# Optimization experiments

Hardware: AMD Instinct MI355X
Metric: run time of the kernel (lower is better)

The kernel has to match this reference:

```python
import jax, jax.numpy as jnp
import numpy as np

B = 16  # graphs per batch; equal-sized graphs per level

def _knn_interpolate(x, pos, pos_skip, k):
    # x: [Ns, C] source feats, pos: [Ns,3], pos_skip: [Nt,3]; B equal-sized graphs.
    Ns, C = x.shape
    Nt = pos_skip.shape[0]
    xs = x.reshape(B, Ns // B, C)
    ps = pos.reshape(B, Ns // B, 3)
    pt = pos_skip.reshape(B, Nt // B, 3)
    def per_graph(xb, pb, qb):
        # squared pairwise distance [nt, ns]
        d2 = (jnp.sum(qb * qb, -1)[:, None] + jnp.sum(pb * pb, -1)[None, :]
              - 2.0 * (qb @ pb.T))
        neg, idx = jax.lax.top_k(-d2, k)          # k smallest distances
        w = 1.0 / jnp.clip(-neg, 1e-16)           # inverse-distance weights [nt,k]
        xg = xb[idx]                               # gather [nt,k,C]
        return jnp.sum(w[..., None] * xg, 1) / jnp.sum(w, 1)[..., None]
    y = jax.vmap(per_graph)(xs, ps, pt)
    return y.reshape(Nt, C)

def _lin(x, W, b):
    return x @ W.T + b

def setup_inputs() -> dict:
    key = jax.random.key(0)
    ks = jax.random.split(key, 24)
    n3, n2, n1, n0 = 1024, 4096, 16384, 65536
    def rn(k, shape, scale=1.0):
        return (jax.random.normal(k, shape, dtype=jnp.float32) * scale)
    inp = {
        'x': rn(ks[0], (n3, 256)),
        'pos': rn(ks[1], (n3, 3)),
        'batch': jnp.repeat(jnp.arange(B), n3 // B),
        'x_skip2': rn(ks[2], (n2, 128)),
        'pos_skip2': rn(ks[3], (n2, 3)),
        'batch2': jnp.repeat(jnp.arange(B), n2 // B),
        'x_skip1': rn(ks[4], (n1, 64)),
        'pos_skip1': rn(ks[5], (n1, 3)),
        'batch1': jnp.repeat(jnp.arange(B), n1 // B),
        'x_skip0': rn(ks[6], (n0, 3)),
        'pos_skip0': rn(ks[7], (n0, 3)),
        'batch0': jnp.repeat(jnp.arange(B), n0 // B),
        # MLP([384,128,128])
        'W3a': rn(ks[8], (128, 384), 384 ** -0.5), 'b3a': jnp.zeros((128,), jnp.float32),
        'W3b': rn(ks[9], (128, 128), 128 ** -0.5), 'b3b': jnp.zeros((128,), jnp.float32),
        # MLP([192,64,64])
        'W2a': rn(ks[10], (64, 192), 192 ** -0.5), 'b2a': jnp.zeros((64,), jnp.float32),
        'W2b': rn(ks[11], (64, 64), 64 ** -0.5), 'b2b': jnp.zeros((64,), jnp.float32),
        # MLP([67,64,64,3])
        'W1a': rn(ks[12], (64, 67), 67 ** -0.5), 'b1a': jnp.zeros((64,), jnp.float32),
        'W1b': rn(ks[13], (64, 64), 64 ** -0.5), 'b1b': jnp.zeros((64,), jnp.float32),
        'W1c': rn(ks[14], (3, 64), 64 ** -0.5), 'b1c': jnp.zeros((3,), jnp.float32),
    }
    return inp

def reference(x, pos, batch, x_skip2, pos_skip2, batch2, x_skip1, pos_skip1, batch1,
              x_skip0, pos_skip0, batch0, W3a, b3a, W3b, b3b, W2a, b2a, W2b, b2b,
              W1a, b1a, W1b, b1b, W1c, b1c):
    # propagate3: k=4, MLP([384,128,128], Tanh, plain last layer)
    h = _knn_interpolate(x, pos, pos_skip2, 4)
    h = jnp.concatenate([h, x_skip2], axis=1)
    h = _lin(jnp.tanh(_lin(h, W3a, b3a)), W3b, b3b)
    # propagate2: k=8, MLP([192,64,64])
    h = _knn_interpolate(h, pos_skip2, pos_skip1, 8)
    h = jnp.concatenate([h, x_skip1], axis=1)
    h = _lin(jnp.tanh(_lin(h, W2a, b2a)), W2b, b2b)
    # propagate1: k=16, MLP([67,64,64,3])
    h = _knn_interpolate(h, pos_skip1, pos_skip0, 16)
    h = jnp.concatenate([h, x_skip0], axis=1)
    h = _lin(jnp.tanh(_lin(jnp.tanh(_lin(h, W1a, b1a)), W1b, b1b)), W1c, b1c)
    return h
```

## Files before the change

kernel.cpp:

```cpp
#include <hip/hip_runtime.h>
#include <math.h>

#define DEV __device__ __forceinline__

typedef unsigned long long u64;
typedef unsigned u32;

DEV u32 fmap(float f) {
    u32 b = __float_as_uint(f);
    return b ^ (u32)(((int)b >> 31) | 0x80000000);
}
DEV float funmap(u32 m) {
    u32 b = (m & 0x80000000u) ? (m ^ 0x80000000u) : ~m;
    return __uint_as_float(b);
}
DEV u32 umin_(u32 a, u32 b) { return __builtin_elementwise_min(a, b); }
DEV u32 umax_(u32 a, u32 b) { return __builtin_elementwise_max(a, b); }

DEV int lane_rank(u64 mask) {
    return (int)__builtin_amdgcn_mbcnt_hi((u32)(mask >> 32),
               __builtin_amdgcn_mbcnt_lo((u32)mask, 0u));
}

DEV float pnorm2(float x, float y, float z) {
    return __fmaf_rn(x, x, __fmaf_rn(y, y, __fmul_rn(z, z)));
}
DEV float qdot(float qx, float qy, float qz, float px, float py, float pz) {
    return __fmaf_rn(qx, px, __fmaf_rn(qy, py, __fmul_rn(qz, pz)));
}
DEV float dist2_core(float qq, float pp, float qp) {
    return __fadd_rn(__fadd_rn(qq, pp), __fmul_rn(-2.f, qp));
}
DEV float dist2(float qx, float qy, float qz, float qq,
                float px, float py, float pz) {
    return dist2_core(qq, pnorm2(px, py, pz), qdot(qx, qy, qz, px, py, pz));
}
DEV float wgt(float d2) { return __builtin_amdgcn_rcpf(fmaxf(d2, 1e-16f)); }

template<int N>
DEV void bitonic_sort(u32 v[N]) {
    #pragma unroll
    for (int k = 2; k <= N; k <<= 1) {
        #pragma unroll
        for (int j = k >> 1; j > 0; j >>= 1) {
            #pragma unroll
            for (int i = 0; i < N; ++i) {
                const int l = i ^ j;
                if (l > i) {
                    const u32 lo = umin_(v[i], v[l]);
                    const u32 hi = umax_(v[i], v[l]);
                    const bool up = ((i & k) == 0);
                    v[i] = up ? lo : hi;
                    v[l] = up ? hi : lo;
                }
            }
        }
    }
}
template<int N>
DEV void bitonic_cleanup(u32 v[N]) {
    #pragma unroll
    for (int j = N >> 1; j > 0; j >>= 1) {
        #pragma unroll
        for (int i = 0; i < N; ++i) {
            const int l = i ^ j;
            if (l > i) {
                const u32 lo = umin_(v[i], v[l]);
                v[l] = umax_(v[i], v[l]);
                v[i] = lo;
            }
        }
    }
}

template<int K, int NSRC, int LOG_TPG, int TPT>
__global__ __launch_bounds__(256) void knn_select(
    const float* __restrict__ pos_s, const float* __restrict__ pos_t,
    u32* __restrict__ Fout)
{
    constexpr int TPB = 256 / TPT;
    constexpr int SL  = NSRC / TPT;
    constexpr int NB  = SL / K;
    constexpr int STRIDE = TPT * K + 1;
    __shared__ float4 sp[NSRC];
    __shared__ u32 lists[TPB * STRIDE];

    const int tid = threadIdx.x;
    const int w = tid / TPT, sub = tid % TPT;
    const int t = blockIdx.x * TPB + w;
    const int g = t >> LOG_TPG, sbase = g * NSRC;

    for (int i = tid; i < NSRC; i += 256) {
        const float* p = pos_s + (size_t)(sbase + i) * 3;
        const float px = p[0], py = p[1], pz = p[2];
        sp[i] = make_float4(px, py, pz, pnorm2(px, py, pz));
    }
    __syncthreads();

    const float qx = pos_t[t*3+0], qy = pos_t[t*3+1], qz = pos_t[t*3+2];
    const float qq = pnorm2(qx, qy, qz);

    u32 r[K];
    #pragma unroll
    for (int j = 0; j < K; ++j) r[j] = 0xFFFFFFFFu;

    for (int b = 0; b < NB; ++b) {
        u32 c[K];
        #pragma unroll
        for (int j = 0; j < K; ++j) {
            const float4 p = sp[(b * K + j) * TPT + sub];
            c[j] = fmap(dist2_core(qq, p.w, qdot(qx, qy, qz, p.x, p.y, p.z)));
        }
        bitonic_sort<K>(c);
        u32 m[K];
        #pragma unroll
        for (int i = 0; i < K; ++i) m[i] = umin_(r[i], c[K-1-i]);
        bitonic_cleanup<K>(m);
        #pragma unroll
        for (int i = 0; i < K; ++i) r[i] = m[i];
    }

    u32* Lw = lists + w * STRIDE;
    #pragma unroll
    for (int j = 0; j < K; ++j) Lw[sub * K + j] = r[j];
    __syncthreads();

    if (sub == 0) {
        u32 h[TPT]; int idx[TPT];
        #pragma unroll
        for (int l = 0; l < TPT; ++l) { h[l] = Lw[l*K]; idx[l] = 1; }
        u32 F = 0;
        #pragma unroll
        for (int step = 0; step < K; ++step) {
            u32 m = h[0];
            #pragma unroll
            for (int l = 1; l < TPT; ++l) m = umin_(m, h[l]);
            F = m;
            if (step < K - 1) {
                bool done = false;
                #pragma unroll
                for (int l = 0; l < TPT; ++l) {
                    if (!done && h[l] == m) {
                        h[l] = (idx[l] < K) ? Lw[l*K + idx[l]] : 0xFFFFFFFFu;
                        ++idx[l];
                        done = true;
                    }
                }
            }
        }
        Fout[t] = F;
    }
}


__global__ __launch_bounds__(512) void knn1_gather(
    const float* __restrict__ xsrc, const float* __restrict__ pos_s,
    const float* __restrict__ pos_t, const float* __restrict__ x_skip,
    const u32* __restrict__ Fbuf, float* __restrict__ out)
{
    constexpr int K = 16, M = 16;
    __shared__ float4 sp[1024];
    __shared__ int2 srw[8 * K];
    const int lane = threadIdx.x & 63;
    const int wv = threadIdx.x >> 6;
    const int t = blockIdx.x * 8 + wv;
    const int g = (blockIdx.x * 8) >> 12;
    const int sbase = g << 10;

    for (int i = threadIdx.x; i < 1024; i += 512) {
        const float* p = pos_s + (size_t)(sbase + i) * 3;
        const float px = p[0], py = p[1], pz = p[2];
        sp[i] = make_float4(px, py, pz, pnorm2(px, py, pz));
    }
    __syncthreads();

    const float qx = pos_t[t*3+0], qy = pos_t[t*3+1], qz = pos_t[t*3+2];
    const float qq = pnorm2(qx, qy, qz);
    float fd[M];
    #pragma unroll
    for (int m = 0; m < M; ++m) {
        const float4 p = sp[lane + m*64];
        fd[m] = dist2_core(qq, p.w, qdot(qx, qy, qz, p.x, p.y, p.z));
    }
    const float Fd = funmap(Fbuf[t]);
    const int base = wv * K;

    int bl = 0, bt = 0; int tr[M];
    #pragma unroll
    for (int m = 0; m < M; ++m) {
        const u64 mlm = __ballot(fd[m] < Fd);
        const u64 mtm = __ballot(fd[m] == Fd);
        if (fd[m] < Fd) {
            const int slot = bl + lane_rank(mlm);
            srw[base + slot] = make_int2(__float_as_int(wgt(fd[m])),
                                         sbase + lane + m*64);
        }
        tr[m] = bt + lane_rank(mtm);
        bl += (int)__popcll(mlm);
        bt += (int)__popcll(mtm);
    }
    const int nless = bl, need = K - nless;
    const float wtie = wgt(Fd);
    #pragma unroll
    for (int m = 0; m < M; ++m) {
        if (fd[m] == Fd && tr[m] < need) {
            srw[base + nless + tr[m]] = make_int2(__float_as_int(wtie),
                                                  sbase + lane + m*64);
        }
    }
    __syncthreads();

    float wsum = 0.f, y = 0.f;
    #pragma unroll
    for (int j = 0; j < K; ++j) {
        const int2 rw = srw[base + j];
        const float w = __int_as_float(rw.x);
        wsum += w;
        y += w * xsrc[(size_t)rw.y * 64 + lane];
    }
    out[t*67 + lane] = y * (1.f / wsum);
    if (lane < 3) out[t*67 + 64 + lane] = x_skip[t*3 + lane];
}

__global__ __launch_bounds__(512) void knn2_gather(
    const float* __restrict__ xsrc, const float* __restrict__ pos_s,
    const float* __restrict__ pos_t, const float* __restrict__ x_skip,
    const u32* __restrict__ Fbuf, float* __restrict__ out)
{
    constexpr int K = 8, M = 4;
    __shared__ float4 sp[256];
    __shared__ int2 srw[8 * K];
    const int lane = threadIdx.x & 63;
    const int wv = threadIdx.x >> 6;
    const int t = blockIdx.x * 8 + wv;
    const int g = (blockIdx.x * 8) >> 10;
    const int sbase = g << 8;

    if (threadIdx.x < 256) {
        const int i = threadIdx.x;
        const float* p = pos_s + (size_t)(sbase + i) * 3;
        const float px = p[0], py = p[1], pz = p[2];
        sp[i] = make_float4(px, py, pz, pnorm2(px, py, pz));
    }
    __syncthreads();

    const float qx = pos_t[t*3+0], qy = pos_t[t*3+1], qz = pos_t[t*3+2];
    const float qq = pnorm2(qx, qy, qz);
    float fd[M];
    #pragma unroll
    for (int m = 0; m < M; ++m) {
        const float4 p = sp[lane + m*64];
        fd[m] = dist2_core(qq, p.w, qdot(qx, qy, qz, p.x, p.y, p.z));
    }
    const float Fd = funmap(Fbuf[t]);
    const int base = wv * K;

    int bl = 0, bt = 0; int tr[M];
    #pragma unroll
    for (int m = 0; m < M; ++m) {
        const u64 mlm = __ballot(fd[m] < Fd);
        const u64 mtm = __ballot(fd[m] == Fd);
        if (fd[m] < Fd) {
            const int slot = bl + lane_rank(mlm);
            srw[base + slot] = make_int2(__float_as_int(wgt(fd[m])),
                                         sbase + lane + m*64);
        }
        tr[m] = bt + lane_rank(mtm);
        bl += (int)__popcll(mlm);
        bt += (int)__popcll(mtm);
    }
    const int nless = bl, need = K - nless;
    const float wtie = wgt(Fd);
    #pragma unroll
    for (int m = 0; m < M; ++m) {
        if (fd[m] == Fd && tr[m] < need) {
            srw[base + nless + tr[m]] = make_int2(__float_as_int(wtie),
                                                  sbase + lane + m*64);
        }
    }
    __syncthreads();

    float wsum = 0.f, y0 = 0.f, y1 = 0.f;
    #pragma unroll
    for (int j = 0; j < K; ++j) {
        const int2 rw = srw[base + j];
        const float w = __int_as_float(rw.x);
        const float* xr = xsrc + (size_t)rw.y * 128;
        wsum += w;
        y0 += w * xr[lane];
        y1 += w * xr[lane + 64];
    }
    const float inv = 1.f / wsum;
    out[t*192 + lane]      = y0 * inv;
    out[t*192 + lane + 64] = y1 * inv;
    out[t*192 + 128 + lane] = x_skip[t*64 + lane];
}

DEV u64 umin64(u64 a, u64 b) { return a < b ? a : b; }
DEV u64 shfl_xor_u64(u64 k, int off) {
    u32 lo = (u32)k, hi = (u32)(k >> 32);
    lo = (u32)__shfl_xor((int)lo, off, 64);
    hi = (u32)__shfl_xor((int)hi, off, 64);
    return ((u64)hi << 32) | lo;
}
DEV u64 wave_min_u64(u64 v) {
    #pragma unroll
    for (int off = 32; off; off >>= 1)
        v = umin64(v, shfl_xor_u64(v, off));
    return v;
}
DEV u64 make_key(float d2, int idx) { return ((u64)fmap(d2) << 10) | (u32)idx; }
DEV float key_weight(u64 k) {
    return __builtin_amdgcn_rcpf(fmaxf(funmap((u32)(k >> 10)), 1e-16f));
}
DEV int key_row(u64 k) {
    return __builtin_amdgcn_readfirstlane((int)((u32)k & 1023u));
}
#define KMAX 0xFFFFFFFFFFFFFFFFull

__global__ __launch_bounds__(256) void knn3_kernel(
    const float* __restrict__ x, const float* __restrict__ pos_s,
    const float* __restrict__ pos_t, const float* __restrict__ x_skip,
    float* __restrict__ out)
{
    const int lane = threadIdx.x & 63;
    const int t = blockIdx.x * 4 + (threadIdx.x >> 6);
    const int g = t >> 8, sbase = g << 6;
    const float qx = pos_t[t*3+0], qy = pos_t[t*3+1], qz = pos_t[t*3+2];
    const float qq = pnorm2(qx, qy, qz);
    const int s = sbase + lane;
    const u64 key = make_key(dist2(qx, qy, qz, qq,
                                   pos_s[s*3+0], pos_s[s*3+1], pos_s[s*3+2]), lane);

    float w[4]; int row[4]; float wsum = 0.f;
    u64 gprev = 0;
    #pragma unroll
    for (int j = 0; j < 4; ++j) {
        gprev = wave_min_u64(key > gprev ? key : KMAX);
        w[j] = key_weight(gprev);
        row[j] = sbase + key_row(gprev);
        wsum += w[j];
    }
    const float inv = 1.f / wsum;
    float y0 = 0.f, y1 = 0.f, y2 = 0.f, y3 = 0.f;
    #pragma unroll
    for (int j = 0; j < 4; ++j) {
        const float* xr = x + (size_t)row[j] * 256;
        y0 += w[j] * xr[lane];
        y1 += w[j] * xr[lane + 64];
        y2 += w[j] * xr[lane + 128];
        y3 += w[j] * xr[lane + 192];
    }
    out[t*384 + lane]       = y0 * inv;
    out[t*384 + lane + 64]  = y1 * inv;
    out[t*384 + lane + 128] = y2 * inv;
    out[t*384 + lane + 192] = y3 * inv;
    out[t*384 + 256 + lane]      = x_skip[t*128 + lane];
    out[t*384 + 256 + 64 + lane] = x_skip[t*128 + 64 + lane];
}

template<int K1, int C1, int C2, int ROWS>
__global__ void mlp2_kernel(
    const float* __restrict__ in, const float* __restrict__ Wa,
    const float* __restrict__ ba, const float* __restrict__ Wb,
    const float* __restrict__ bb, float* __restrict__ out, int N)
{
    __shared__ float xt[ROWS * K1];
    __shared__ float h1[ROWS * C1];
    const int tid = threadIdx.x;
    const int row0 = blockIdx.x * ROWS;

    for (int f = tid; f < ROWS * K1; f += C1)
        xt[f] = in[row0 * K1 + f];
    __syncthreads();

    float acc[ROWS];
    #pragma unroll
    for (int r = 0; r < ROWS; ++r) acc[r] = ba[tid];
    for (int k = 0; k < K1; ++k) {
        const float wv = Wa[tid * K1 + k];
        #pragma unroll
        for (int r = 0; r < ROWS; ++r) acc[r] += xt[r * K1 + k] * wv;
    }
    #pragma unroll
    for (int r = 0; r < ROWS; ++r) h1[r * C1 + tid] = tanhf(acc[r]);
    __syncthreads();

    if (tid < C2) {
        float acc2[ROWS];
        #pragma unroll
        for (int r = 0; r < ROWS; ++r) acc2[r] = bb[tid];
        for (int k = 0; k < C1; ++k) {
            const float wv = Wb[tid * C1 + k];
            #pragma unroll
            for (int r = 0; r < ROWS; ++r) acc2[r] += h1[r * C1 + k] * wv;
        }
        #pragma unroll
        for (int r = 0; r < ROWS; ++r) out[(row0 + r) * C2 + tid] = acc2[r];
    }
}

template<int ROWS>
__global__ __launch_bounds__(256) void mlp_final_kernel(
    const float* __restrict__ in,
    const float* __restrict__ Wa, const float* __restrict__ ba,
    const float* __restrict__ Wb, const float* __restrict__ bb,
    const float* __restrict__ Wc, const float* __restrict__ bc,
    float* __restrict__ out, int N)
{
    constexpr int K1 = 67, C = 64;
    __shared__ float xt[4][ROWS * K1];
    __shared__ float h1[4][ROWS * C];
    __shared__ float h2[4][ROWS * 65];
    const int tid = threadIdx.x & 63;
    const int wv = threadIdx.x >> 6;
    const int row0 = (blockIdx.x * 4 + wv) * ROWS;

    for (int f = tid; f < ROWS * K1; f += C)
        xt[wv][f] = in[row0 * K1 + f];
    __syncthreads();

    float acc[ROWS];
    #pragma unroll
    for (int r = 0; r < ROWS; ++r) acc[r] = ba[tid];
    for (int k = 0; k < K1; ++k) {
        const float wvv = Wa[tid * K1 + k];
        #pragma unroll
        for (int r = 0; r < ROWS; ++r) acc[r] += xt[wv][r * K1 + k] * wvv;
    }
    #pragma unroll
    for (int r = 0; r < ROWS; ++r) h1[wv][r * C + tid] = tanhf(acc[r]);
    __syncthreads();

    float acc2[ROWS];
    #pragma unroll
    for (int r = 0; r < ROWS; ++r) acc2[r] = bb[tid];
    for (int k = 0; k < C; ++k) {
        const float wvv = Wb[tid * C + k];
        #pragma unroll
        for (int r = 0; r < ROWS; ++r) acc2[r] += h1[wv][r * C + k] * wvv;
    }
    #pragma unroll
    for (int r = 0; r < ROWS; ++r) h2[wv][r * 65 + tid] = tanhf(acc2[r]);
    __syncthreads();

    if (tid < ROWS * 3) {
        const int r = tid / 3, o = tid - r * 3;
        float a = bc[o];
        for (int k = 0; k < C; ++k) a += h2[wv][r * 65 + k] * Wc[o * C + k];
        out[(row0 + r) * 3 + o] = a;
    }
}

extern "C" void kernel_launch(void* const* d_in, const int* in_sizes, int n_in,
                              void* d_out, int out_size, void* d_ws, size_t ws_size,
                              hipStream_t stream)
{
    const float* x       = (const float*)d_in[0];
    const float* pos     = (const float*)d_in[1];
    const float* x_skip2 = (const float*)d_in[3];
    const float* pos2    = (const float*)d_in[4];
    const float* x_skip1 = (const float*)d_in[6];
    const float* pos1    = (const float*)d_in[7];
    const float* x_skip0 = (const float*)d_in[9];
    const float* pos0    = (const float*)d_in[10];
    const float* W3a = (const float*)d_in[12]; const float* b3a = (const float*)d_in[13];
    const float* W3b = (const float*)d_in[14]; const float* b3b = (const float*)d_in[15];
    const float* W2a = (const float*)d_in[16]; const float* b2a = (const float*)d_in[17];
    const float* W2b = (const float*)d_in[18]; const float* b2b = (const float*)d_in[19];
    const float* W1a = (const float*)d_in[20]; const float* b1a = (const float*)d_in[21];
    const float* W1b = (const float*)d_in[22]; const float* b1b = (const float*)d_in[23];
    const float* W1c = (const float*)d_in[24]; const float* b1c = (const float*)d_in[25];

    float* buf1 = (float*)d_ws;
    float* buf2 = buf1 + (size_t)65536 * 67;
    u32*   F1   = (u32*)(buf2 + (size_t)16384 * 64);
    u32*   F2   = F1 + 65536;

    knn3_kernel<<<1024, 256, 0, stream>>>(x, pos, pos2, x_skip2, buf1);
    mlp2_kernel<384,128,128,8><<<4096/8, 128, 0, stream>>>(buf1, W3a, b3a, W3b, b3b, buf2, 4096);
    knn_select<8, 256, 10, 4><<<16384/64, 256, 0, stream>>>(pos2, pos1, F2);
    knn2_gather<<<16384/8, 512, 0, stream>>>(buf2, pos2, pos1, x_skip1, F2, buf1);
    mlp2_kernel<192,64,64,8><<<16384/8, 64, 0, stream>>>(buf1, W2a, b2a, W2b, b2b, buf2, 16384);
    knn_select<16, 1024, 12, 4><<<65536/64, 256, 0, stream>>>(pos1, pos0, F1);
    knn1_gather<<<65536/8, 512, 0, stream>>>(buf2, pos1, pos0, x_skip0, F1, buf1);
    mlp_final_kernel<8><<<65536/32, 256, 0, stream>>>(buf1, W1a, b1a, W1b, b1b, W1c, b1c,
                                                      (float*)d_out, 65536);
}
```

Measured before the change: 209.9 us.

## Emit neighbor index/weight rows from kNN select; simplify gather kernels

The select kernel now re-scans its source points after finding the k-th distance threshold and writes the (weight, index) rows for each target directly to global memory, with tie handling via per-thread counts and a serial fallback. The gather kernels then only read these rows and accumulate features, no longer reloading positions or recomputing distances with ballots. This removes the duplicated distance pass and shared-memory staging from the gather kernels. In exchange it adds a second and third distance pass inside select, extra syncs, and global writes and reads of the row buffers.

Measured after the change: 284.0 us. 35.3% more time.

```diff
diff --git a/kernel.cpp b/kernel.cpp
--- a/kernel.cpp
+++ b/kernel.cpp
@@ -16,11 +16,6 @@
 }
 DEV u32 umin_(u32 a, u32 b) { return __builtin_elementwise_min(a, b); }
 DEV u32 umax_(u32 a, u32 b) { return __builtin_elementwise_max(a, b); }
-
-DEV int lane_rank(u64 mask) {
-    return (int)__builtin_amdgcn_mbcnt_hi((u32)(mask >> 32),
-               __builtin_amdgcn_mbcnt_lo((u32)mask, 0u));
-}
 
 DEV float pnorm2(float x, float y, float z) {
     return __fmaf_rn(x, x, __fmaf_rn(y, y, __fmul_rn(z, z)));
@@ -74,9 +69,9 @@
 }
 
 template<int K, int NSRC, int LOG_TPG, int TPT>
-__global__ __launch_bounds__(256) void knn_select(
+__global__ __launch_bounds__(256) void knn_select_emit(
     const float* __restrict__ pos_s, const float* __restrict__ pos_t,
-    u32* __restrict__ Fout)
+    int2* __restrict__ rows)
 {
     constexpr int TPB = 256 / TPT;
     constexpr int SL  = NSRC / TPT;
@@ -84,6 +79,9 @@
     constexpr int STRIDE = TPT * K + 1;
     __shared__ float4 sp[NSRC];
     __shared__ u32 lists[TPB * STRIDE];
+    __shared__ u32 Fsh[TPB];
+    __shared__ int cnts[TPB * TPT];
+    __shared__ int tcnts[TPB * TPT];
 
     const int tid = threadIdx.x;
     const int w = tid / TPT, sub = tid % TPT;
@@ -148,72 +146,74 @@
                 }
             }
         }
-        Fout[t] = F;
+        Fsh[w] = F;
+    }
+    __syncthreads();
+    const u32 F = Fsh[w];
+
+    int cnt = 0, tcnt = 0;
+    for (int s = 0; s < SL; ++s) {
+        const float4 p = sp[s * TPT + sub];
+        const u32 key = fmap(dist2_core(qq, p.w, qdot(qx, qy, qz, p.x, p.y, p.z)));
+        cnt  += (key < F);
+        tcnt += (key == F);
+    }
+    cnts[w*TPT + sub] = cnt; tcnts[w*TPT + sub] = tcnt;
+    __syncthreads();
+
+    int pre = 0, nless = 0, tpre = 0, tall = 0;
+    #pragma unroll
+    for (int l = 0; l < TPT; ++l) {
+        const int c = cnts[w*TPT + l], tc = tcnts[w*TPT + l];
+        if (l < sub) { pre += c; tpre += tc; }
+        nless += c; tall += tc;
+    }
+    const int need = K - nless;
+    const float wtie = wgt(funmap(F));
+    const bool tfast = (tall == need);
+    int2* rt = rows + (size_t)t * K;
+
+    int slot = pre;
+    int ts = nless + tpre;
+    for (int s = 0; s < SL; ++s) {
+        const float4 p = sp[s * TPT + sub];
+        const float d2 = dist2_core(qq, p.w, qdot(qx, qy, qz, p.x, p.y, p.z));
+        const u32 key = fmap(d2);
+        const int gi = sbase + s * TPT + sub;
+        if (key < F) {
+            rt[slot] = make_int2(__float_as_int(wgt(d2)), gi);
+            ++slot;
+        } else if (tfast && key == F) {
+            rt[ts] = make_int2(__float_as_int(wtie), gi);
+            ++ts;
+        }
+    }
+    if (!tfast && sub == 0) {
+        int rc = 0;
+        for (int gi2 = 0; gi2 < NSRC && rc < need; ++gi2) {
+            const float4 p = sp[gi2];
+            const u32 key = fmap(dist2_core(qq, p.w, qdot(qx, qy, qz, p.x, p.y, p.z)));
+            if (key == F) {
+                rt[nless + rc] = make_int2(__float_as_int(wtie), sbase + gi2);
+                ++rc;
+            }
+        }
     }
 }
 
 
 __global__ __launch_bounds__(512) void knn1_gather(
-    const float* __restrict__ xsrc, const float* __restrict__ pos_s,
-    const float* __restrict__ pos_t, const float* __restrict__ x_skip,
-    const u32* __restrict__ Fbuf, float* __restrict__ out)
-{
-    constexpr int K = 16, M = 16;
-    __shared__ float4 sp[1024];
-    __shared__ int2 srw[8 * K];
+    const float* __restrict__ xsrc, const int2* __restrict__ rows,
+    const float* __restrict__ x_skip, float* __restrict__ out)
+{
+    constexpr int K = 16;
     const int lane = threadIdx.x & 63;
-    const int wv = threadIdx.x >> 6;
-    const int t = blockIdx.x * 8 + wv;
-    const int g = (blockIdx.x * 8) >> 12;
-    const int sbase = g << 10;
-
-    for (int i = threadIdx.x; i < 1024; i += 512) {
-        const float* p = pos_s + (size_t)(sbase + i) * 3;
-        const float px = p[0], py = p[1], pz = p[2];
-        sp[i] = make_float4(px, py, pz, pnorm2(px, py, pz));
-    }
-    __syncthreads();
-
-    const float qx = pos_t[t*3+0], qy = pos_t[t*3+1], qz = pos_t[t*3+2];
-    const float qq = pnorm2(qx, qy, qz);
-    float fd[M];
-    #pragma unroll
-    for (int m = 0; m < M; ++m) {
-        const float4 p = sp[lane + m*64];
-        fd[m] = dist2_core(qq, p.w, qdot(qx, qy, qz, p.x, p.y, p.z));
-    }
-    const float Fd = funmap(Fbuf[t]);
-    const int base = wv * K;
-
-    int bl = 0, bt = 0; int tr[M];
-    #pragma unroll
-    for (int m = 0; m < M; ++m) {
-        const u64 mlm = __ballot(fd[m] < Fd);
-        const u64 mtm = __ballot(fd[m] == Fd);
-        if (fd[m] < Fd) {
-            const int slot = bl + lane_rank(mlm);
-            srw[base + slot] = make_int2(__float_as_int(wgt(fd[m])),
-                                         sbase + lane + m*64);
-        }
-        tr[m] = bt + lane_rank(mtm);
-        bl += (int)__popcll(mlm);
-        bt += (int)__popcll(mtm);
-    }
-    const int nless = bl, need = K - nless;
-    const float wtie = wgt(Fd);
-    #pragma unroll
-    for (int m = 0; m < M; ++m) {
-        if (fd[m] == Fd && tr[m] < need) {
-            srw[base + nless + tr[m]] = make_int2(__float_as_int(wtie),
-                                                  sbase + lane + m*64);
-        }
-    }
-    __syncthreads();
-
+    const int t = blockIdx.x * 8 + (threadIdx.x >> 6);
+    const int2* rt = rows + (size_t)t * K;
     float wsum = 0.f, y = 0.f;
     #pragma unroll
     for (int j = 0; j < K; ++j) {
-        const int2 rw = srw[base + j];
+        const int2 rw = rt[j];
         const float w = __int_as_float(rw.x);
         wsum += w;
         y += w * xsrc[(size_t)rw.y * 64 + lane];
@@ -223,67 +223,17 @@
 }
 
 __global__ __launch_bounds__(512) void knn2_gather(
-    const float* __restrict__ xsrc, const float* __restrict__ pos_s,
-    const float* __restrict__ pos_t, const float* __restrict__ x_skip,
-    const u32* __restrict__ Fbuf, float* __restrict__ out)
-{
-    constexpr int K = 8, M = 4;
-    __shared__ float4 sp[256];
-    __shared__ int2 srw[8 * K];
+    const float* __restrict__ xsrc, const int2* __restrict__ rows,
+    const float* __restrict__ x_skip, float* __restrict__ out)
+{
+    constexpr int K = 8;
     const int lane = threadIdx.x & 63;
-    const int wv = threadIdx.x >> 6;
-    const int t = blockIdx.x * 8 + wv;
-    const int g = (blockIdx.x * 8) >> 10;
-    const int sbase = g << 8;
-
-    if (threadIdx.x < 256) {
-        const int i = threadIdx.x;
-        const float* p = pos_s + (size_t)(sbase + i) * 3;
-        const float px = p[0], py = p[1], pz = p[2];
-        sp[i] = make_float4(px, py, pz, pnorm2(px, py, pz));
-    }
-    __syncthreads();
-
-    const float qx = pos_t[t*3+0], qy = pos_t[t*3+1], qz = pos_t[t*3+2];
-    const float qq = pnorm2(qx, qy, qz);
-    float fd[M];
-    #pragma unroll
-    for (int m = 0; m < M; ++m) {
-        const float4 p = sp[lane + m*64];
-        fd[m] = dist2_core(qq, p.w, qdot(qx, qy, qz, p.x, p.y, p.z));
-    }
-    const float Fd = funmap(Fbuf[t]);
-    const int base = wv * K;
-
-    int bl = 0, bt = 0; int tr[M];
-    #pragma unroll
-    for (int m = 0; m < M; ++m) {
-        const u64 mlm = __ballot(fd[m] < Fd);
-        const u64 mtm = __ballot(fd[m] == Fd);
-        if (fd[m] < Fd) {
-            const int slot = bl + lane_rank(mlm);
-            srw[base + slot] = make_int2(__float_as_int(wgt(fd[m])),
-                                         sbase + lane + m*64);
-        }
-        tr[m] = bt + lane_rank(mtm);
-        bl += (int)__popcll(mlm);
-        bt += (int)__popcll(mtm);
-    }
-    const int nless = bl, need = K - nless;
-    const float wtie = wgt(Fd);
-    #pragma unroll
-    for (int m = 0; m < M; ++m) {
-        if (fd[m] == Fd && tr[m] < need) {
-            srw[base + nless + tr[m]] = make_int2(__float_as_int(wtie),
-                                                  sbase + lane + m*64);
-        }
-    }
-    __syncthreads();
-
+    const int t = blockIdx.x * 8 + (threadIdx.x >> 6);
+    const int2* rt = rows + (size_t)t * K;
     float wsum = 0.f, y0 = 0.f, y1 = 0.f;
     #pragma unroll
     for (int j = 0; j < K; ++j) {
-        const int2 rw = srw[base + j];
+        const int2 rw = rt[j];
         const float w = __int_as_float(rw.x);
         const float* xr = xsrc + (size_t)rw.y * 128;
         wsum += w;
@@ -474,16 +424,16 @@
 
     float* buf1 = (float*)d_ws;
     float* buf2 = buf1 + (size_t)65536 * 67;
-    u32*   F1   = (u32*)(buf2 + (size_t)16384 * 64);
-    u32*   F2   = F1 + 65536;
+    int2*  rows1 = (int2*)(buf2 + (size_t)16384 * 64);
+    int2*  rows2 = rows1 + (size_t)65536 * 16;
 
     knn3_kernel<<<1024, 256, 0, stream>>>(x, pos, pos2, x_skip2, buf1);
     mlp2_kernel<384,128,128,8><<<4096/8, 128, 0, stream>>>(buf1, W3a, b3a, W3b, b3b, buf2, 4096);
-    knn_select<8, 256, 10, 4><<<16384/64, 256, 0, stream>>>(pos2, pos1, F2);
-    knn2_gather<<<16384/8, 512, 0, stream>>>(buf2, pos2, pos1, x_skip1, F2, buf1);
+    knn_select_emit<8, 256, 10, 4><<<16384/64, 256, 0, stream>>>(pos2, pos1, rows2);
+    knn2_gather<<<16384/8, 512, 0, stream>>>(buf2, rows2, x_skip1, buf1);
     mlp2_kernel<192,64,64,8><<<16384/8, 64, 0, stream>>>(buf1, W2a, b2a, W2b, b2b, buf2, 16384);
-    knn_select<16, 1024, 12, 4><<<65536/64, 256, 0, stream>>>(pos1, pos0, F1);
-    knn1_gather<<<65536/8, 512, 0, stream>>>(buf2, pos1, pos0, x_skip0, F1, buf1);
+    knn_select_emit<16, 1024, 12, 4><<<65536/64, 256, 0, stream>>>(pos1, pos0, rows1);
+    knn1_gather<<<65536/8, 512, 0, stream>>>(buf2, rows1, x_skip0, buf1);
     mlp_final_kernel<8><<<65536/32, 256, 0, stream>>>(buf1, W1a, b1a, W1b, b1b, W1c, b1c,
                                                       (float*)d_out, 65536);
 }
```
